# Kernel optimization log

Measured on AMD Instinct MI355X. Metric: run time of the kernel, lower is better.

The kernel has to match this reference:

```python
import jax, jax.numpy as jnp
import numpy as np

N = 8192
IN_F = 256
OUT_F = 256


def setup_inputs() -> dict:
    key = jax.random.key(0)
    k1, k2, k3 = jax.random.split(key, 3)
    x = jax.random.normal(k1, (N, IN_F), dtype=jnp.float32)
    adj = jax.random.randint(k2, (N, N), 0, 2, dtype=jnp.int32)
    # glorot-uniform init over last two dims of (3, 2F, O)
    stdv = float(np.sqrt(6.0 / (2 * IN_F + OUT_F)))
    weight = jax.random.uniform(k3, (3, 2 * IN_F, OUT_F), dtype=jnp.float32,
                                minval=-stdv, maxval=stdv)
    bias = jnp.zeros((OUT_F,), dtype=jnp.float32)
    return {"g": 0, "x": x, "adj": adj, "weight": weight, "bias": bias}


def reference(g, x, adj, weight, bias):
    # per-node mean over neighbors: vectorized replacement of the python loop
    mask = (adj == 1).astype(x.dtype)               # [N, N]
    deg = jnp.sum(mask, axis=1, keepdims=True)      # [N, 1]
    x1 = (mask @ x) / deg                           # [N, F] mean aggregate
    n_x = jnp.concatenate([x1, x], axis=1)          # [N, 2F]
    # [N,2F] x [3,2F,O] broadcasts to [3,N,O]
    out = jnp.einsum('nf,kfo->kno', n_x, weight) + bias
    return out
```

## Files before the change

### kernel.cpp

```cpp
#include <hip/hip_runtime.h>


typedef unsigned short u16;
typedef int   i32x4 __attribute__((ext_vector_type(4)));
typedef unsigned u32x4 __attribute__((ext_vector_type(4)));
typedef float f32x4 __attribute__((ext_vector_type(4)));

__device__ __forceinline__ u16 f2b(float f) {
  unsigned u = __builtin_bit_cast(unsigned, f);
  return (u16)((u + 0x7FFFu + ((u >> 16) & 1u)) >> 16);
}
__device__ __forceinline__ unsigned pack2(float a, float b) {
  return (unsigned)f2b(a) | ((unsigned)f2b(b) << 16);
}
__device__ __forceinline__ f32x4 mfma16(u32x4 a, u32x4 b, f32x4 c) {
  asm("v_mfma_f32_16x16x32_bf16 %0, %1, %2, %0" : "+v"(c) : "v"(a), "v"(b));
  return c;
}

__global__ __launch_bounds__(256) void conv_xtf(const float* __restrict__ x,
                                                u16* __restrict__ xtf) {
  int c = blockIdx.x * 256 + threadIdx.x;
  int kc8 = c >> 8, f = c & 255;
  const float* p = x + (size_t)kc8 * 2048 + f;
  u32x4 h;
  h.x = pack2(p[0],    p[256]);
  h.y = pack2(p[512],  p[768]);
  h.z = pack2(p[1024], p[1280]);
  h.w = pack2(p[1536], p[1792]);
  *(u32x4*)(xtf + (size_t)c * 8) = h;
}

__global__ __launch_bounds__(256) void conv_nx(const float* __restrict__ x,
                                               u16* __restrict__ nxtf) {
  int c = blockIdx.x * 256 + threadIdx.x;
  int kc8r = c >> 13, m = c & 8191;
  const float* p = x + (size_t)m * 256 + kc8r * 8;
  f32x4 p0 = *(const f32x4*)p;
  f32x4 p1 = *(const f32x4*)(p + 4);
  u32x4 h;
  h.x = pack2(p0.x, p0.y); h.y = pack2(p0.z, p0.w);
  h.z = pack2(p1.x, p1.y); h.w = pack2(p1.z, p1.w);
  *(u32x4*)(nxtf + ((size_t)(32 + kc8r) * 8192 + m) * 8) = h;
}

__global__ __launch_bounds__(768) void conv_w(const float* __restrict__ w,
                                              u16* __restrict__ wtf) {
  int kc8 = blockIdx.x;
  int c = threadIdx.x;
  int kk = c >> 8, o = c & 255;
  const float* p = w + (size_t)kk * 131072 + (size_t)kc8 * 2048 + o;
  u32x4 h;
  h.x = pack2(p[0],    p[256]);
  h.y = pack2(p[512],  p[768]);
  h.z = pack2(p[1024], p[1280]);
  h.w = pack2(p[1536], p[1792]);
  *(u32x4*)(wtf + ((size_t)kc8 * 768 + c) * 8) = h;
}

__global__ __launch_bounds__(1024) void phase1(const int* __restrict__ adj,
                                               const u16* __restrict__ xtf,
                                               u16* __restrict__ nxtf) {
  __shared__ __align__(16) u16 AsmF[4 * 32 * 72];
  __shared__ float Csum[32 * 260];
  __shared__ int degs[1024];
  __shared__ float degrow[32];

  const int t  = threadIdx.x;
  const int g  = t >> 8;
  const int lt = t & 255;
  const int l  = t & 63;
  const int w4 = lt >> 6;
  const int l15 = l & 15, l16 = l >> 4;
  const int m0 = blockIdx.x * 32;
  const int r = lt >> 3, kq = lt & 7;

  f32x4 acc[2][4] = {};
  int dsum = 0;

  const int* arow = adj + (size_t)(m0 + r) * 8192 + g * 2048 + kq * 8;
  const int afrag0 = (g * 32 + l15) * 72 + l16 * 8;
  const u16* bbase = xtf + (size_t)l16 * 2048 + (size_t)(w4 * 64 + l15) * 8;

  for (int step = 0; step < 32; ++step) {
    const int k0 = g * 2048 + step * 64;
    __syncthreads();
    i32x4 p0 = __builtin_nontemporal_load((const i32x4*)(arow + step * 64));
    i32x4 p1 = __builtin_nontemporal_load((const i32x4*)(arow + step * 64) + 1);
    dsum += p0.x + p0.y + p0.z + p0.w + p1.x + p1.y + p1.z + p1.w;
    u32x4 h;
    h.x = (p0.x ? 0x3F80u : 0u) | (p0.y ? 0x3F800000u : 0u);
    h.y = (p0.z ? 0x3F80u : 0u) | (p0.w ? 0x3F800000u : 0u);
    h.z = (p1.x ? 0x3F80u : 0u) | (p1.y ? 0x3F800000u : 0u);
    h.w = (p1.z ? 0x3F80u : 0u) | (p1.w ? 0x3F800000u : 0u);
    *(u32x4*)&AsmF[(g * 32 + r) * 72 + kq * 8] = h;
    __syncthreads();
    const u16* bstep = bbase + ((size_t)k0 << 8);
#pragma unroll
    for (int kc = 0; kc < 2; ++kc) {
      u32x4 a0 = *(const u32x4*)&AsmF[afrag0 + kc * 32];
      u32x4 a1 = *(const u32x4*)&AsmF[afrag0 + 16 * 72 + kc * 32];
#pragma unroll
      for (int nt = 0; nt < 4; ++nt) {
        u32x4 b = *(const u32x4*)(bstep + kc * 8192 + nt * 128);
        acc[0][nt] = mfma16(a0, b, acc[0][nt]);
        acc[1][nt] = mfma16(a1, b, acc[1][nt]);
      }
    }
  }
  asm volatile("s_nop 7\n\ts_nop 7\n\ts_nop 7");

  degs[t] = dsum;
  __syncthreads();
  if (t < 32) {
    int s = 0;
#pragma unroll
    for (int gg = 0; gg < 4; ++gg)
#pragma unroll
      for (int j = 0; j < 8; ++j) s += degs[gg * 256 + t * 8 + j];
    degrow[t] = (float)s;
  }
  for (int gg = 0; gg < 4; ++gg) {
    if (g == gg) {
#pragma unroll
      for (int mt = 0; mt < 2; ++mt)
#pragma unroll
        for (int nt = 0; nt < 4; ++nt)
#pragma unroll
          for (int i = 0; i < 4; ++i) {
            int row = mt * 16 + l16 * 4 + i;
            int col = w4 * 64 + nt * 16 + l15;
            if (gg == 0) Csum[row * 260 + col] = acc[mt][nt][i];
            else         Csum[row * 260 + col] += acc[mt][nt][i];
          }
    }
    __syncthreads();
  }
  {
    int rr = t & 31, kc8 = t >> 5;
    float rd = 1.0f / degrow[rr];
    const float* cp = &Csum[rr * 260 + kc8 * 8];
    u32x4 h;
    h.x = pack2(cp[0] * rd, cp[1] * rd);
    h.y = pack2(cp[2] * rd, cp[3] * rd);
    h.z = pack2(cp[4] * rd, cp[5] * rd);
    h.w = pack2(cp[6] * rd, cp[7] * rd);
    *(u32x4*)(nxtf + ((size_t)kc8 * 8192 + m0 + rr) * 8) = h;
  }
}

__global__ __launch_bounds__(256) void phase2(const u16* __restrict__ nxtf,
                                              const u16* __restrict__ wtf,
                                              const float* __restrict__ bias,
                                              float* __restrict__ out) {
  const int t = threadIdx.x, l = t & 63, w = t >> 6;
  const int wm = w & 1, wn = w >> 1;
  const int l15 = l & 15, l16 = l >> 4;
  const int m0 = blockIdx.x * 128, c0 = blockIdx.y * 96;
  f32x4 acc[4][3] = {};
  const u16* abase = nxtf + (size_t)l16 * 65536 + (size_t)(m0 + wm * 64 + l15) * 8;
  const u16* bbase = wtf  + (size_t)l16 * 6144  + (size_t)(c0 + wn * 48 + l15) * 8;
  float bv[3];
#pragma unroll
  for (int nt = 0; nt < 3; ++nt) bv[nt] = bias[(c0 + wn * 48 + nt * 16 + l15) & 255];
#pragma unroll 2
  for (int step = 0; step < 16; ++step) {
    u32x4 a[4], b[3];
#pragma unroll
    for (int mt = 0; mt < 4; ++mt)
      a[mt] = *(const u32x4*)(abase + (size_t)step * 262144 + mt * 128);
#pragma unroll
    for (int nt = 0; nt < 3; ++nt)
      b[nt] = *(const u32x4*)(bbase + (size_t)step * 24576 + nt * 128);
#pragma unroll
    for (int mt = 0; mt < 4; ++mt)
#pragma unroll
      for (int nt = 0; nt < 3; ++nt)
        acc[mt][nt] = mfma16(a[mt], b[nt], acc[mt][nt]);
  }
  asm volatile("s_nop 7\n\ts_nop 7\n\ts_nop 7");
#pragma unroll
  for (int mt = 0; mt < 4; ++mt)
#pragma unroll
    for (int nt = 0; nt < 3; ++nt) {
      int c = c0 + wn * 48 + nt * 16 + l15;
      int kk = c >> 8, o = c & 255;
      float* op = out + (size_t)kk * 2097152 +
                  (size_t)(m0 + wm * 64 + mt * 16 + l16 * 4) * 256 + o;
#pragma unroll
      for (int i = 0; i < 4; ++i)
        __builtin_nontemporal_store(acc[mt][nt][i] + bv[nt], op + (size_t)i * 256);
    }
}

extern "C" void kernel_launch(void* const* d_in, const int* in_sizes, int n_in,
                              void* d_out, int out_size, void* d_ws, size_t ws_size,
                              hipStream_t stream) {
  (void)in_sizes; (void)n_in; (void)out_size; (void)ws_size;
  const float* x    = (const float*)d_in[1];
  const int*   adj  = (const int*)d_in[2];
  const float* wgt  = (const float*)d_in[3];
  const float* bias = (const float*)d_in[4];
  float* out = (float*)d_out;

  char* ws = (char*)d_ws;
  u16* xtf  = (u16*)ws;
  u16* nxtf = (u16*)(ws + (4u << 20));
  u16* wtf  = (u16*)(ws + (12u << 20));

  conv_xtf<<<1024, 256, 0, stream>>>(x, xtf);
  conv_nx <<<1024, 256, 0, stream>>>(x, nxtf);
  conv_w  <<<64, 768, 0, stream>>>(wgt, wtf);
  phase1  <<<256, 1024, 0, stream>>>(adj, xtf, nxtf);
  phase2  <<<dim3(64, 8), 256, 0, stream>>>(nxtf, wtf, bias, out);
}
```

Before: 435.8 us.

## Double-buffer adjacency tiles in phase1 and merge conversion kernels into one launch

Phase1 now keeps two LDS buffers for the adjacency mask tile. It prefetches the next step's adjacency loads into registers while computing MFMAs on the current buffer, which cuts the syncs from two per step to one. The three bf16 conversion kernels are merged into a single launch with block-range dispatch to remove two kernel launch overheads. The cost is more LDS and register use per block, which could lower occupancy.

```diff
diff --git a/kernel.cpp b/kernel.cpp
--- a/kernel.cpp
+++ b/kernel.cpp
@@ -18,50 +18,51 @@
   return c;
 }
 
-__global__ __launch_bounds__(256) void conv_xtf(const float* __restrict__ x,
-                                                u16* __restrict__ xtf) {
-  int c = blockIdx.x * 256 + threadIdx.x;
-  int kc8 = c >> 8, f = c & 255;
-  const float* p = x + (size_t)kc8 * 2048 + f;
-  u32x4 h;
-  h.x = pack2(p[0],    p[256]);
-  h.y = pack2(p[512],  p[768]);
-  h.z = pack2(p[1024], p[1280]);
-  h.w = pack2(p[1536], p[1792]);
-  *(u32x4*)(xtf + (size_t)c * 8) = h;
-}
-
-__global__ __launch_bounds__(256) void conv_nx(const float* __restrict__ x,
-                                               u16* __restrict__ nxtf) {
-  int c = blockIdx.x * 256 + threadIdx.x;
-  int kc8r = c >> 13, m = c & 8191;
-  const float* p = x + (size_t)m * 256 + kc8r * 8;
-  f32x4 p0 = *(const f32x4*)p;
-  f32x4 p1 = *(const f32x4*)(p + 4);
-  u32x4 h;
-  h.x = pack2(p0.x, p0.y); h.y = pack2(p0.z, p0.w);
-  h.z = pack2(p1.x, p1.y); h.w = pack2(p1.z, p1.w);
-  *(u32x4*)(nxtf + ((size_t)(32 + kc8r) * 8192 + m) * 8) = h;
-}
-
-__global__ __launch_bounds__(768) void conv_w(const float* __restrict__ w,
-                                              u16* __restrict__ wtf) {
-  int kc8 = blockIdx.x;
-  int c = threadIdx.x;
-  int kk = c >> 8, o = c & 255;
-  const float* p = w + (size_t)kk * 131072 + (size_t)kc8 * 2048 + o;
-  u32x4 h;
-  h.x = pack2(p[0],    p[256]);
-  h.y = pack2(p[512],  p[768]);
-  h.z = pack2(p[1024], p[1280]);
-  h.w = pack2(p[1536], p[1792]);
-  *(u32x4*)(wtf + ((size_t)kc8 * 768 + c) * 8) = h;
+__global__ __launch_bounds__(256) void conv_all(const float* __restrict__ x,
+                                                const float* __restrict__ w,
+                                                u16* __restrict__ xtf,
+                                                u16* __restrict__ nxtf,
+                                                u16* __restrict__ wtf) {
+  const int b = blockIdx.x;
+  if (b < 1024) {
+    int c = b * 256 + threadIdx.x;
+    int kc8 = c >> 8, f = c & 255;
+    const float* p = x + (size_t)kc8 * 2048 + f;
+    u32x4 h;
+    h.x = pack2(p[0],    p[256]);
+    h.y = pack2(p[512],  p[768]);
+    h.z = pack2(p[1024], p[1280]);
+    h.w = pack2(p[1536], p[1792]);
+    *(u32x4*)(xtf + (size_t)c * 8) = h;
+  } else if (b < 2048) {
+    int c = (b - 1024) * 256 + threadIdx.x;
+    int kc8r = c >> 13, m = c & 8191;
+    const float* p = x + (size_t)m * 256 + kc8r * 8;
+    f32x4 p0 = *(const f32x4*)p;
+    f32x4 p1 = *(const f32x4*)(p + 4);
+    u32x4 h;
+    h.x = pack2(p0.x, p0.y); h.y = pack2(p0.z, p0.w);
+    h.z = pack2(p1.x, p1.y); h.w = pack2(p1.z, p1.w);
+    *(u32x4*)(nxtf + ((size_t)(32 + kc8r) * 8192 + m) * 8) = h;
+  } else {
+    int idx = (b - 2048) * 256 + threadIdx.x;
+    int kc8 = idx / 768;
+    int c = idx - kc8 * 768;
+    int kk = c >> 8, o = c & 255;
+    const float* p = w + (size_t)kk * 131072 + (size_t)kc8 * 2048 + o;
+    u32x4 h;
+    h.x = pack2(p[0],    p[256]);
+    h.y = pack2(p[512],  p[768]);
+    h.z = pack2(p[1024], p[1280]);
+    h.w = pack2(p[1536], p[1792]);
+    *(u32x4*)(wtf + (size_t)idx * 8) = h;
+  }
 }
 
 __global__ __launch_bounds__(1024) void phase1(const int* __restrict__ adj,
                                                const u16* __restrict__ xtf,
                                                u16* __restrict__ nxtf) {
-  __shared__ __align__(16) u16 AsmF[4 * 32 * 72];
+  __shared__ __align__(16) u16 AsmF[2][4 * 32 * 72];
   __shared__ float Csum[32 * 260];
   __shared__ int degs[1024];
   __shared__ float degrow[32];
@@ -79,27 +80,30 @@
   int dsum = 0;
 
   const int* arow = adj + (size_t)(m0 + r) * 8192 + g * 2048 + kq * 8;
+  u16* const stp0 = &AsmF[0][(g * 32 + r) * 72 + kq * 8];
+  u16* const stp1 = &AsmF[1][(g * 32 + r) * 72 + kq * 8];
   const int afrag0 = (g * 32 + l15) * 72 + l16 * 8;
   const u16* bbase = xtf + (size_t)l16 * 2048 + (size_t)(w4 * 64 + l15) * 8;
 
-  for (int step = 0; step < 32; ++step) {
-    const int k0 = g * 2048 + step * 64;
-    __syncthreads();
-    i32x4 p0 = __builtin_nontemporal_load((const i32x4*)(arow + step * 64));
-    i32x4 p1 = __builtin_nontemporal_load((const i32x4*)(arow + step * 64) + 1);
+  auto LOADA = [&](i32x4& d0, i32x4& d1, int s) {
+    d0 = __builtin_nontemporal_load((const i32x4*)(arow + s * 64));
+    d1 = __builtin_nontemporal_load((const i32x4*)(arow + s * 64) + 1);
+  };
+  auto CONVST = [&](i32x4 p0, i32x4 p1, u16* stp) {
     dsum += p0.x + p0.y + p0.z + p0.w + p1.x + p1.y + p1.z + p1.w;
     u32x4 h;
     h.x = (p0.x ? 0x3F80u : 0u) | (p0.y ? 0x3F800000u : 0u);
     h.y = (p0.z ? 0x3F80u : 0u) | (p0.w ? 0x3F800000u : 0u);
     h.z = (p1.x ? 0x3F80u : 0u) | (p1.y ? 0x3F800000u : 0u);
     h.w = (p1.z ? 0x3F80u : 0u) | (p1.w ? 0x3F800000u : 0u);
-    *(u32x4*)&AsmF[(g * 32 + r) * 72 + kq * 8] = h;
-    __syncthreads();
-    const u16* bstep = bbase + ((size_t)k0 << 8);
+    *(u32x4*)stp = h;
+  };
+  auto COMPUTE = [&](int s, int buf) {
+    const u16* bstep = bbase + ((size_t)(g * 2048 + s * 64) << 8);
 #pragma unroll
     for (int kc = 0; kc < 2; ++kc) {
-      u32x4 a0 = *(const u32x4*)&AsmF[afrag0 + kc * 32];
-      u32x4 a1 = *(const u32x4*)&AsmF[afrag0 + 16 * 72 + kc * 32];
+      u32x4 a0 = *(const u32x4*)&AsmF[buf][afrag0 + kc * 32];
+      u32x4 a1 = *(const u32x4*)&AsmF[buf][afrag0 + 16 * 72 + kc * 32];
 #pragma unroll
       for (int nt = 0; nt < 4; ++nt) {
         u32x4 b = *(const u32x4*)(bstep + kc * 8192 + nt * 128);
@@ -107,18 +111,40 @@
         acc[1][nt] = mfma16(a1, b, acc[1][nt]);
       }
     }
-  }
+  };
+
+  i32x4 pa0, pa1, pb0, pb1;
+  LOADA(pa0, pa1, 0);
+  CONVST(pa0, pa1, stp0);
+  LOADA(pb0, pb1, 1);
+  __syncthreads();
+
+  for (int it = 0; it < 15; ++it) {
+    const int s = it * 2;
+    LOADA(pa0, pa1, s + 2);
+    COMPUTE(s, 0);
+    CONVST(pb0, pb1, stp1);
+    __syncthreads();
+    LOADA(pb0, pb1, s + 3);
+    COMPUTE(s + 1, 1);
+    CONVST(pa0, pa1, stp0);
+    __syncthreads();
+  }
+  COMPUTE(30, 0);
+  CONVST(pb0, pb1, stp1);
+  __syncthreads();
+  COMPUTE(31, 1);
   asm volatile("s_nop 7\n\ts_nop 7\n\ts_nop 7");
 
   degs[t] = dsum;
   __syncthreads();
   if (t < 32) {
-    int s = 0;
+    int sum = 0;
 #pragma unroll
     for (int gg = 0; gg < 4; ++gg)
 #pragma unroll
-      for (int j = 0; j < 8; ++j) s += degs[gg * 256 + t * 8 + j];
-    degrow[t] = (float)s;
+      for (int j = 0; j < 8; ++j) sum += degs[gg * 256 + t * 8 + j];
+    degrow[t] = (float)sum;
   }
   for (int gg = 0; gg < 4; ++gg) {
     if (g == gg) {
@@ -208,9 +234,7 @@
   u16* nxtf = (u16*)(ws + (4u << 20));
   u16* wtf  = (u16*)(ws + (12u << 20));
 
-  conv_xtf<<<1024, 256, 0, stream>>>(x, xtf);
-  conv_nx <<<1024, 256, 0, stream>>>(x, nxtf);
-  conv_w  <<<64, 768, 0, stream>>>(wgt, wtf);
+  conv_all<<<2240, 256, 0, stream>>>(x, wgt, xtf, nxtf, wtf);
   phase1  <<<256, 1024, 0, stream>>>(adj, xtf, nxtf);
   phase2  <<<dim3(64, 8), 256, 0, stream>>>(nxtf, wtf, bias, out);
 }
```

New measurement: 421.7 us (median of 2 runs). -3.2%, faster.
